# Kernel tuning notes

Measured on AMD Instinct MI355X. Metric: run time of the kernel, lower is better.

The kernel has to match this reference:

```python
import jax, jax.numpy as jnp
import numpy as np


def setup_inputs() -> dict:
    key = jax.random.key(0)
    k1, k2 = jax.random.split(key)
    B, C, H, W, K = 8, 32, 224, 224, 5
    x = jax.random.normal(k1, (B, C, H, W), dtype=jnp.float32)
    kernel = jax.random.normal(k2, (C, 1, K, K), dtype=jnp.float32) * 0.1
    return {"x": x, "kernel": kernel, "stride": 1, "padding": 2, "dilation": 1}


def reference(x, kernel, stride, padding, dilation):
    # Tropical-max (morphological dilation) conv: out[p] = max_k (x[p+k] + w_flipped[k]).
    # is_max=True, softmax_temp=None -> hard max; kernel is flipped (true convolution).
    B, C, H, W = x.shape
    OC, _, K, _ = kernel.shape
    neutral = -jnp.inf
    x_pad = jnp.pad(x, ((0, 0), (0, 0), (padding, padding), (padding, padding)),
                    constant_values=neutral)
    Hp, Wp = H + 2 * padding, W + 2 * padding
    H_out = (Hp - dilation * (K - 1) - 1) // stride + 1
    W_out = (Wp - dilation * (K - 1) - 1) // stride + 1
    wflip = kernel[:, 0, ::-1, ::-1]  # (C, K, K) flipped, as in torch kernel.flip((2,3))
    # Start from neutral: matches the extra neutral row padded onto the unfold tensor.
    out = jnp.full((B, C, H_out, W_out), neutral, dtype=x.dtype)
    for i in range(K):  # small fixed K*K loop; avoids materializing the (B,C,K^2,HW) unfold
        for j in range(K):
            patch = x_pad[:, :,
                          i * dilation: i * dilation + (H_out - 1) * stride + 1: stride,
                          j * dilation: j * dilation + (W_out - 1) * stride + 1: stride]
            out = jnp.maximum(out, patch + wflip[:, i, j][None, :, None, None])
    return out
```

## Files before the change

kernel.cpp:

```cpp
#include <hip/hip_runtime.h>
#include <math.h>


#define TC_B 8
#define TC_C 32
#define TC_H 224
#define TC_W 224
#define TC_WQ 56
#define TC_HG 14
#define T_ROWS 20
#define ROW_F4 65
#define ROW_FL (ROW_F4 * 4)
#define NWG (TC_B * TC_C * TC_HG)
#define NXCD 8
#define WPX (NWG / NXCD)

typedef float f4v __attribute__((ext_vector_type(4)));

__global__ __launch_bounds__(256) void tropical_conv2d_kernel(
    const float* __restrict__ x, const float* __restrict__ kern,
    float* __restrict__ out) {
  const int tid = threadIdx.x;
  const int lane = tid & 63;
  const int yl = tid >> 6;

  const int orig = blockIdx.x;
  const int blk = (orig & (NXCD - 1)) * WPX + (orig >> 3);

  const int hg = blk % TC_HG;
  const int bc = blk / TC_HG;
  const int c = bc & (TC_C - 1);

  __shared__ float tile[T_ROWS * ROW_FL];

  const float NEG = -INFINITY;
  const float4 NINF4 = make_float4(NEG, NEG, NEG, NEG);
  const float* xp = x + (size_t)bc * (TC_H * TC_W);

  if (tid < T_ROWS) *(float4*)&tile[tid * ROW_FL] = NINF4;

  const int cl = lane < TC_WQ ? lane : TC_WQ - 1;
  #pragma unroll
  for (int rr = 0; rr < 5; ++rr) {
    const int r = yl * 5 + rr;
    const int g = hg * 16 - 2 + r;
    float* ldsrow = &tile[r * ROW_FL + 4];
    if (g >= 0 && g < TC_H) {
      const float* gp = xp + (size_t)g * TC_W + cl * 4;
      __builtin_amdgcn_global_load_lds(
          (const __attribute__((address_space(1))) void*)gp,
          (__attribute__((address_space(3))) void*)ldsrow, 16, 0, 0);
    } else {
      *(float4*)(ldsrow + (size_t)lane * 4) = NINF4;
    }
  }

  float w[25];
  #pragma unroll
  for (int q = 0; q < 25; ++q) w[q] = kern[c * 25 + 24 - q];

  __syncthreads();

  if (lane >= TC_WQ) return;

  const int hbase = hg * 16 + yl * 4;

  float acc[4][4];
  #pragma unroll
  for (int o = 0; o < 4; ++o)
    #pragma unroll
    for (int k = 0; k < 4; ++k) acc[o][k] = NEG;

  const bool redge = (lane == TC_WQ - 1);

  #pragma unroll
  for (int ri = 0; ri < 8; ++ri) {
    const float* rp = &tile[(yl * 4 + ri) * ROW_FL + 4 * lane];
    const float4 A = *(const float4*)(rp);
    const float4 Bv = *(const float4*)(rp + 4);
    const float4 Cv = *(const float4*)(rp + 8);
    float v[12] = {A.x, A.y, A.z, A.w, Bv.x, Bv.y, Bv.z, Bv.w,
                   Cv.x, Cv.y, Cv.z, Cv.w};
    v[8] = redge ? NEG : v[8];
    v[9] = redge ? NEG : v[9];

    #pragma unroll
    for (int o = 0; o < 4; ++o) {
      const int i = ri - o;
      if (i < 0 || i > 4) continue;
      #pragma unroll
      for (int k = 0; k < 4; ++k) {
        const float t0 = v[2 + k] + w[i * 5 + 0];
        const float t1 = v[3 + k] + w[i * 5 + 1];
        const float t2 = v[4 + k] + w[i * 5 + 2];
        const float t3 = v[5 + k] + w[i * 5 + 3];
        const float t4 = v[6 + k] + w[i * 5 + 4];
        acc[o][k] = fmaxf(fmaxf(fmaxf(t0, t1), t2),
                          fmaxf(fmaxf(t3, t4), acc[o][k]));
      }
    }
  }

  float* op = out + (size_t)bc * (TC_H * TC_W) + (size_t)hbase * TC_W;
  #pragma unroll
  for (int o = 0; o < 4; ++o) {
    f4v val = {acc[o][0], acc[o][1], acc[o][2], acc[o][3]};
    __builtin_nontemporal_store(val, (f4v*)(op + (size_t)o * TC_W) + lane);
  }
}

extern "C" void kernel_launch(void* const* d_in, const int* in_sizes, int n_in,
                              void* d_out, int out_size, void* d_ws, size_t ws_size,
                              hipStream_t stream) {
  const float* x = (const float*)d_in[0];
  const float* k = (const float*)d_in[1];
  float* out = (float*)d_out;

  dim3 block(256, 1, 1);
  dim3 grid(NWG, 1, 1);
  tropical_conv2d_kernel<<<grid, block, 0, stream>>>(x, k, out);
}
```

Measured before the change: 111.8 us.

## Process two 16-row output tiles per block, overlapping second-half staging with compute

Each workgroup now covers 32 output rows instead of 16, halving the grid. It stages 36 input rows, which cuts the halo overhead. The last 16 input rows are loaded asynchronously into LDS while the first 16 output rows are computed, with a barrier before computing the second half. This reduces redundant halo loads and hides part of the global-to-LDS latency, at the cost of fewer workgroups, more LDS per block and an extra sync.

```diff
diff --git a/kernel.cpp b/kernel.cpp
--- a/kernel.cpp
+++ b/kernel.cpp
@@ -7,8 +7,8 @@
 #define TC_H 224
 #define TC_W 224
 #define TC_WQ 56
-#define TC_HG 14
-#define T_ROWS 20
+#define TC_HG 7
+#define T_ROWS 36
 #define ROW_F4 65
 #define ROW_FL (ROW_F4 * 4)
 #define NWG (TC_B * TC_C * TC_HG)
@@ -17,65 +17,34 @@
 
 typedef float f4v __attribute__((ext_vector_type(4)));
 
-__global__ __launch_bounds__(256) void tropical_conv2d_kernel(
-    const float* __restrict__ x, const float* __restrict__ kern,
-    float* __restrict__ out) {
-  const int tid = threadIdx.x;
-  const int lane = tid & 63;
-  const int yl = tid >> 6;
+__device__ __forceinline__ void stage_row_16B(
+    const float* __restrict__ xp, float* tile, int r, int g, int cl, int lane) {
+  const float NEG = -INFINITY;
+  float* ldsrow = &tile[r * ROW_FL + 4];
+  if (g >= 0 && g < TC_H) {
+    const float* gp = xp + (size_t)g * TC_W + cl * 4;
+    __builtin_amdgcn_global_load_lds(
+        (const __attribute__((address_space(1))) void*)gp,
+        (__attribute__((address_space(3))) void*)ldsrow, 16, 0, 0);
+  } else {
+    *(float4*)(ldsrow + (size_t)lane * 4) =
+        make_float4(NEG, NEG, NEG, NEG);
+  }
+}
 
-  const int orig = blockIdx.x;
-  const int blk = (orig & (NXCD - 1)) * WPX + (orig >> 3);
-
-  const int hg = blk % TC_HG;
-  const int bc = blk / TC_HG;
-  const int c = bc & (TC_C - 1);
-
-  __shared__ float tile[T_ROWS * ROW_FL];
-
+__device__ __forceinline__ void compute_store_tile(
+    const float* tile, const float* w, float* op_base,
+    int trow_base, int lane, bool redge) {
   const float NEG = -INFINITY;
-  const float4 NINF4 = make_float4(NEG, NEG, NEG, NEG);
-  const float* xp = x + (size_t)bc * (TC_H * TC_W);
-
-  if (tid < T_ROWS) *(float4*)&tile[tid * ROW_FL] = NINF4;
-
-  const int cl = lane < TC_WQ ? lane : TC_WQ - 1;
-  #pragma unroll
-  for (int rr = 0; rr < 5; ++rr) {
-    const int r = yl * 5 + rr;
-    const int g = hg * 16 - 2 + r;
-    float* ldsrow = &tile[r * ROW_FL + 4];
-    if (g >= 0 && g < TC_H) {
-      const float* gp = xp + (size_t)g * TC_W + cl * 4;
-      __builtin_amdgcn_global_load_lds(
-          (const __attribute__((address_space(1))) void*)gp,
-          (__attribute__((address_space(3))) void*)ldsrow, 16, 0, 0);
-    } else {
-      *(float4*)(ldsrow + (size_t)lane * 4) = NINF4;
-    }
-  }
-
-  float w[25];
-  #pragma unroll
-  for (int q = 0; q < 25; ++q) w[q] = kern[c * 25 + 24 - q];
-
-  __syncthreads();
-
-  if (lane >= TC_WQ) return;
-
-  const int hbase = hg * 16 + yl * 4;
-
   float acc[4][4];
   #pragma unroll
   for (int o = 0; o < 4; ++o)
     #pragma unroll
     for (int k = 0; k < 4; ++k) acc[o][k] = NEG;
 
-  const bool redge = (lane == TC_WQ - 1);
-
   #pragma unroll
   for (int ri = 0; ri < 8; ++ri) {
-    const float* rp = &tile[(yl * 4 + ri) * ROW_FL + 4 * lane];
+    const float* rp = &tile[(trow_base + ri) * ROW_FL + 4 * lane];
     const float4 A = *(const float4*)(rp);
     const float4 Bv = *(const float4*)(rp + 4);
     const float4 Cv = *(const float4*)(rp + 8);
@@ -101,11 +70,70 @@
     }
   }
 
-  float* op = out + (size_t)bc * (TC_H * TC_W) + (size_t)hbase * TC_W;
   #pragma unroll
   for (int o = 0; o < 4; ++o) {
     f4v val = {acc[o][0], acc[o][1], acc[o][2], acc[o][3]};
-    __builtin_nontemporal_store(val, (f4v*)(op + (size_t)o * TC_W) + lane);
+    __builtin_nontemporal_store(val, (f4v*)(op_base + (size_t)o * TC_W) + lane);
+  }
+}
+
+__global__ __launch_bounds__(256) void tropical_conv2d_kernel(
+    const float* __restrict__ x, const float* __restrict__ kern,
+    float* __restrict__ out) {
+  const int tid = threadIdx.x;
+  const int lane = tid & 63;
+  const int yl = tid >> 6;
+
+  const int orig = blockIdx.x;
+  const int blk = (orig & (NXCD - 1)) * WPX + (orig >> 3);
+
+  const int hg = blk % TC_HG;
+  const int bc = blk / TC_HG;
+  const int c = bc & (TC_C - 1);
+
+  __shared__ float tile[T_ROWS * ROW_FL];
+
+  const float NEG = -INFINITY;
+  const float4 NINF4 = make_float4(NEG, NEG, NEG, NEG);
+  const float* xp = x + (size_t)bc * (TC_H * TC_W);
+  const int g0 = hg * 32 - 2;
+
+  if (tid < T_ROWS) *(float4*)&tile[tid * ROW_FL] = NINF4;
+
+  const int cl = lane < TC_WQ ? lane : TC_WQ - 1;
+
+  #pragma unroll
+  for (int rr = 0; rr < 5; ++rr) {
+    const int r = yl * 5 + rr;
+    stage_row_16B(xp, tile, r, g0 + r, cl, lane);
+  }
+
+  float w[25];
+  #pragma unroll
+  for (int q = 0; q < 25; ++q) w[q] = kern[c * 25 + 24 - q];
+
+  __syncthreads();
+
+  #pragma unroll
+  for (int rr = 0; rr < 4; ++rr) {
+    const int r = 20 + yl * 4 + rr;
+    stage_row_16B(xp, tile, r, g0 + r, cl, lane);
+  }
+
+  const bool active = (lane < TC_WQ);
+  const bool redge = (lane == TC_WQ - 1);
+  float* opb = out + (size_t)bc * (TC_H * TC_W);
+
+  if (active) {
+    compute_store_tile(tile, w, opb + (size_t)(hg * 32 + yl * 4) * TC_W,
+                       yl * 4, lane, redge);
+  }
+
+  __syncthreads();
+
+  if (active) {
+    compute_store_tile(tile, w, opb + (size_t)(hg * 32 + 16 + yl * 4) * TC_W,
+                       16 + yl * 4, lane, redge);
   }
 }
 
```

Result: slower. 116.0 us (+3.8%).
